# Performance work log

Measured on AMD Instinct MI355X. Metric: run time of the kernel, lower is better.

Reference implementation:

```python
import jax, jax.numpy as jnp
import numpy as np

D_MODEL = 1024
NHEAD = 16
HEAD_DIM = D_MODEL // NHEAD
B, T = 2, 2048


def setup_inputs() -> dict:
    key = jax.random.key(0)
    ks = jax.random.split(key, 11)
    s = 1.0 / np.sqrt(D_MODEL)
    inp = {
        'q': jax.random.normal(ks[0], (B, T, D_MODEL), jnp.float32),
        'k': jax.random.normal(ks[1], (B, T, D_MODEL), jnp.float32),
        'v': jax.random.normal(ks[2], (B, T, D_MODEL), jnp.float32),
        'Wq': jax.random.normal(ks[3], (D_MODEL, D_MODEL), jnp.float32) * s,
        'bq': jnp.zeros((D_MODEL,), jnp.float32),
        'Wk': jax.random.normal(ks[4], (D_MODEL, D_MODEL), jnp.float32) * s,
        'bk': jnp.zeros((D_MODEL,), jnp.float32),
        'Wv': jax.random.normal(ks[5], (D_MODEL, D_MODEL), jnp.float32) * s,
        'bv': jnp.zeros((D_MODEL,), jnp.float32),
        'Wo': jax.random.normal(ks[6], (D_MODEL, D_MODEL), jnp.float32) * s,
        'bo': jnp.zeros((D_MODEL,), jnp.float32),
    }
    return inp


def reference(q, k, v, Wq, bq, Wk, bk, Wv, bv, Wo, bo):
    scale = np.sqrt(HEAD_DIM).astype(np.float32)
    # projections (torch Linear: x @ W.T + b), split heads -> [B, H, T, Dh]
    def proj(x, W, b):
        y = jnp.einsum('btd,ed->bte', x, W) + b
        return y.reshape(B, T, NHEAD, HEAD_DIM).transpose(0, 2, 1, 3)
    qh = proj(q, Wq, bq)
    kh = proj(k, Wk, bk)
    vh = proj(v, Wv, bv)
    scores = jnp.einsum('bhqd,bhkd->bhqk', qh, kh) / scale  # [B,H,T,T]
    weights = jax.nn.softmax(scores, axis=-1)
    out = jnp.einsum('bhqk,bhkd->bhqd', weights, vh)        # [B,H,T,Dh]
    out = out.transpose(0, 2, 1, 3).reshape(B, T, D_MODEL)
    return jnp.einsum('btd,ed->bte', out, Wo) + bo
```

## Files before the change

kernel.cpp:

```cpp
#include <hip/hip_runtime.h>
#include <cstdint>
#include <cstddef>


#define D_MODEL 1024
#define NHEAD   16
#define HDIM    64
#define BATCH   2
#define SEQ     2048
#define BT      (BATCH * SEQ)

#define QSCALE 0.18033688011112043f

typedef __bf16 bf16;
typedef __bf16 bf16x8 __attribute__((ext_vector_type(8)));
typedef __bf16 bf16x4 __attribute__((ext_vector_type(4)));
typedef float  floatx4 __attribute__((ext_vector_type(4)));
typedef short  short4v __attribute__((ext_vector_type(4)));

#define MFMA16(a, b, c) __builtin_amdgcn_mfma_f32_16x16x32_bf16((a), (b), (c), 0, 0, 0)

__device__ __forceinline__ floatx4 MFMA16B(bf16x4 a, bf16x4 b, floatx4 c) {
  return __builtin_amdgcn_mfma_f32_16x16x16bf16_1k(
      __builtin_bit_cast(short4v, a), __builtin_bit_cast(short4v, b), c, 0, 0, 0);
}

__device__ __forceinline__ float fexp2(float x) {
  return __builtin_amdgcn_exp2f(x);
}

__device__ __forceinline__ void async_cp16(const bf16* g, bf16* l) {
  __builtin_amdgcn_global_load_lds(
      (__attribute__((address_space(1))) void*)(g),
      (__attribute__((address_space(3))) void*)(l), 16, 0, 0);
}

__global__ __launch_bounds__(256) void cvt7(
    const float* __restrict__ s0, const float* __restrict__ s1,
    const float* __restrict__ s2, const float* __restrict__ s3,
    const float* __restrict__ s4, const float* __restrict__ s5,
    const float* __restrict__ s6,
    bf16* __restrict__ d0, bf16* __restrict__ d1, bf16* __restrict__ d2,
    bf16* __restrict__ d3, bf16* __restrict__ d4, bf16* __restrict__ d5,
    bf16* __restrict__ d6)
{
  const float* src; bf16* dst; int n4;
  switch (blockIdx.y) {
    case 0:  src = s0; dst = d0; n4 = (BT * D_MODEL) / 4; break;
    case 1:  src = s1; dst = d1; n4 = (BT * D_MODEL) / 4; break;
    case 2:  src = s2; dst = d2; n4 = (BT * D_MODEL) / 4; break;
    case 3:  src = s3; dst = d3; n4 = (D_MODEL * D_MODEL) / 4; break;
    case 4:  src = s4; dst = d4; n4 = (D_MODEL * D_MODEL) / 4; break;
    case 5:  src = s5; dst = d5; n4 = (D_MODEL * D_MODEL) / 4; break;
    default: src = s6; dst = d6; n4 = (D_MODEL * D_MODEL) / 4; break;
  }
  int stride = gridDim.x * blockDim.x;
  for (int i = blockIdx.x * blockDim.x + threadIdx.x; i < n4; i += stride) {
    float4 f = ((const float4*)src)[i];
    bf16x4 h;
    h[0] = (bf16)f.x; h[1] = (bf16)f.y; h[2] = (bf16)f.z; h[3] = (bf16)f.w;
    ((bf16x4*)dst)[i] = h;
  }
}

__device__ __forceinline__ void gemm128_core(
    const bf16* __restrict__ A, const bf16* __restrict__ W,
    int m0, int n0, bf16* As, bf16* Bs, floatx4 acc[4][4])
{
  const int t = threadIdx.x;
  const int l = t & 63, w = t >> 6;
  const int quad = l >> 4, lr = l & 15;
  const int wm = (w >> 1) * 64, wn = (w & 1) * 64;

  floatx4 z = {0.f, 0.f, 0.f, 0.f};
#pragma unroll
  for (int i = 0; i < 4; i++)
#pragma unroll
    for (int j = 0; j < 4; j++) acc[i][j] = z;

  for (int kt = 0; kt < 1024; kt += 32) {
    __syncthreads();
#pragma unroll
    for (int i = 0; i < 2; i++) {
      int c = i * 256 + t;
      int row = c >> 2, ci = c & 3;
      async_cp16(A + (size_t)(m0 + row) * 1024 + kt + ci * 8,
                 As + (i * 256 + w * 64) * 8);
      async_cp16(W + (size_t)(n0 + row) * 1024 + kt + ci * 8,
                 Bs + (i * 256 + w * 64) * 8);
    }
    __syncthreads();

    bf16x8 af[4], bfr[4];
#pragma unroll
    for (int i = 0; i < 4; i++) {
      af[i]  = *(const bf16x8*)(As + (wm + i * 16 + lr) * 32 + quad * 8);
      bfr[i] = *(const bf16x8*)(Bs + (wn + i * 16 + lr) * 32 + quad * 8);
    }
#pragma unroll
    for (int i = 0; i < 4; i++)
#pragma unroll
      for (int j = 0; j < 4; j++)
        acc[i][j] = MFMA16(af[i], bfr[j], acc[i][j]);
  }
}

__global__ __launch_bounds__(256) void qkv_gemm(
    const bf16* __restrict__ qb, const bf16* __restrict__ kb, const bf16* __restrict__ vb,
    const bf16* __restrict__ wq, const bf16* __restrict__ wk, const bf16* __restrict__ wv,
    const float* __restrict__ biasq, const float* __restrict__ biask, const float* __restrict__ biasv,
    bf16* __restrict__ qh, bf16* __restrict__ kh, bf16* __restrict__ vt)
{
  __shared__ bf16 As[128 * 32];
  __shared__ bf16 Bs[128 * 32];
  const int zid = blockIdx.z;
  const bf16* A = (zid == 0) ? qb : ((zid == 1) ? kb : vb);
  const bf16* W = (zid == 0) ? wq : ((zid == 1) ? wk : wv);
  const float* bias = (zid == 0) ? biasq : ((zid == 1) ? biask : biasv);
  const int m0 = blockIdx.x * 128, n0 = blockIdx.y * 128;

  floatx4 acc[4][4];
  gemm128_core(A, W, m0, n0, As, Bs, acc);

  const int t = threadIdx.x, l = t & 63, w = t >> 6;
  const int quad = l >> 4, lr = l & 15;
  const int wm = (w >> 1) * 64, wn = (w & 1) * 64;
  const float sc = (zid == 0) ? QSCALE : 1.0f;

  if (zid < 2) {
    bf16* out = (zid == 0) ? qh : kh;
#pragma unroll
    for (int i = 0; i < 4; i++) {
      int mbase = m0 + wm + i * 16 + quad * 4;
      int b  = mbase >> 11;
      int tq = mbase & 2047;
#pragma unroll
      for (int j = 0; j < 4; j++) {
        int n = n0 + wn + j * 16 + lr;
        float bv = bias[n];
        int h = n >> 6, dh = n & 63;
        bf16* p = out + ((size_t)((b * NHEAD + h) * SEQ + tq)) * HDIM + dh;
#pragma unroll
        for (int r = 0; r < 4; r++)
          p[(size_t)r * HDIM] = (bf16)((acc[i][j][r] + bv) * sc);
      }
    }
  } else {
#pragma unroll
    for (int i = 0; i < 4; i++) {
      int mbase = m0 + wm + i * 16 + quad * 4;
      int b  = mbase >> 11;
      int tq = mbase & 2047;
#pragma unroll
      for (int j = 0; j < 4; j++) {
        int n = n0 + wn + j * 16 + lr;
        float bv = bias[n];
        int h = n >> 6, dh = n & 63;
        bf16x4 pk;
#pragma unroll
        for (int r = 0; r < 4; r++) pk[r] = (bf16)(acc[i][j][r] + bv);
        *(bf16x4*)(vt + ((size_t)((b * NHEAD + h) * HDIM + dh)) * SEQ + tq) = pk;
      }
    }
  }
}

__global__ __launch_bounds__(256, 2) void attn_fused(
    const bf16* __restrict__ qh, const bf16* __restrict__ kh,
    const bf16* __restrict__ vt, bf16* __restrict__ attn)
{
  __shared__ __align__(16) char smem[65536];

  const int t = threadIdx.x, l = t & 63, w = t >> 6;
  const int quad = l >> 4, lr = l & 15;
  const int bh = blockIdx.y;
  const int qt0 = blockIdx.x * 128;
  const bf16* qg = qh + (size_t)bh * SEQ * HDIM;
  const bf16* kg = kh + (size_t)bh * SEQ * HDIM;
  const bf16* vg = vt + (size_t)bh * HDIM * SEQ;

  const bf16* kseg[4];
  const bf16* vseg[4];
#pragma unroll
  for (int i = 0; i < 4; i++) {
    int s = w * 4 + i;
    int krow = s * 8 + (l >> 3);
    kseg[i] = kg + (size_t)krow * HDIM + (((l & 7) ^ (l >> 3)) * 8);
    int vrow = s * 4 + (l >> 4);
    vseg[i] = vg + (size_t)vrow * SEQ + (((l & 15) ^ (vrow & 15)) * 8);
  }

  bf16x8 qf[2][2];
#pragma unroll
  for (int g = 0; g < 2; g++)
#pragma unroll
    for (int ko = 0; ko < 2; ko++)
      qf[g][ko] = *(const bf16x8*)(qg + (size_t)(qt0 + w * 32 + g * 16 + lr) * HDIM
                                   + ko * 32 + quad * 8);

  const floatx4 zz = {0.f, 0.f, 0.f, 0.f};
  floatx4 Oacc[2][4];
#pragma unroll
  for (int g = 0; g < 2; g++)
#pragma unroll
    for (int dt = 0; dt < 4; dt++) Oacc[g][dt] = zz;
  float mrow[2] = {-3.0e38f, -3.0e38f};
  float lrow[2] = {0.f, 0.f};

  auto stage = [&](int buf, int kt) {
    bf16* Kb = (bf16*)(smem + buf * 32768);
    bf16* Vb = (bf16*)(smem + buf * 32768 + 16384);
    int off = kt * 128;
#pragma unroll
    for (int i = 0; i < 4; i++) {
      async_cp16(kseg[i] + (size_t)off * HDIM, Kb + (w * 4 + i) * 512);
      async_cp16(vseg[i] + off,                Vb + (w * 4 + i) * 512);
    }
  };

  stage(0, 0);

  for (int kt = 0; kt < 16; kt++) {
    const int p = kt & 1;
    __syncthreads();
    if (kt + 1 < 16) stage(1 - p, kt + 1);
    const bf16* Ks  = (const bf16*)(smem + p * 32768);
    const bf16* Vts = (const bf16*)(smem + p * 32768 + 16384);

    const bf16* krow0 = Ks + lr * 64 + ((quad ^ (lr & 7)) * 8);
    const bf16* krow1 = Ks + lr * 64 + (((quad + 4) ^ (lr & 7)) * 8);

    floatx4 s0[8], s1[8];
#pragma unroll
    for (int ni = 0; ni < 8; ni++) {
      bf16x8 k0 = *(const bf16x8*)(krow0 + ni * 1024);
      bf16x8 k1 = *(const bf16x8*)(krow1 + ni * 1024);
      floatx4 a0 = MFMA16(k0, qf[0][0], zz);
      a0 = MFMA16(k1, qf[0][1], a0);
      floatx4 a1 = MFMA16(k0, qf[1][0], zz);
      a1 = MFMA16(k1, qf[1][1], a1);
      s0[ni] = a0;
      s1[ni] = a1;
    }

    bf16x4 pk0[8], pk1[8];
#pragma unroll
    for (int g = 0; g < 2; g++) {
      floatx4* sg = g ? s1 : s0;
      bf16x4* pkg = g ? pk1 : pk0;
      float rmax = sg[0][0];
#pragma unroll
      for (int ni = 0; ni < 8; ni++)
#pragma unroll
        for (int r = 0; r < 4; r++) rmax = fmaxf(rmax, sg[ni][r]);
      rmax = fmaxf(rmax, __shfl_xor(rmax, 16, 64));
      rmax = fmaxf(rmax, __shfl_xor(rmax, 32, 64));
      if (!__all(rmax - mrow[g] <= 8.0f)) {
        float mnew = fmaxf(mrow[g], rmax);
        float al = fexp2(mrow[g] - mnew);
        mrow[g] = mnew;
        lrow[g] *= al;
#pragma unroll
        for (int dt = 0; dt < 4; dt++)
#pragma unroll
          for (int r = 0; r < 4; r++) Oacc[g][dt][r] *= al;
      }
      float m = mrow[g];
      float rsum = 0.f;
#pragma unroll
      for (int ni = 0; ni < 8; ni++)
#pragma unroll
        for (int r = 0; r < 4; r++) {
          float pv = fexp2(sg[ni][r] - m);
          rsum += pv;
          pkg[ni][r] = (bf16)pv;
        }
      rsum += __shfl_xor(rsum, 16, 64);
      rsum += __shfl_xor(rsum, 32, 64);
      lrow[g] += rsum;
    }

    const bf16* vbase = Vts + lr * 128 + (quad & 1) * 4;
#pragma unroll
    for (int ni = 0; ni < 8; ni++) {
      const bf16* vp = vbase + (((ni * 2 + (quad >> 1)) ^ lr) * 8);
#pragma unroll
      for (int dt = 0; dt < 4; dt++) {
        bf16x4 vf = *(const bf16x4*)(vp + dt * 2048);
        Oacc[0][dt] = MFMA16B(vf, pk0[ni], Oacc[0][dt]);
        Oacc[1][dt] = MFMA16B(vf, pk1[ni], Oacc[1][dt]);
      }
    }
  }

  bf16* Ost = (bf16*)smem;
#pragma unroll
  for (int g = 0; g < 2; g++) {
    float inv = 1.0f / lrow[g];
#pragma unroll
    for (int dt = 0; dt < 4; dt++) {
      bf16x4 ov;
#pragma unroll
      for (int r = 0; r < 4; r++) ov[r] = (bf16)(Oacc[g][dt][r] * inv);
      *(bf16x4*)(Ost + (size_t)(w * 32 + g * 16 + lr) * 72 + dt * 16 + quad * 4) = ov;
    }
  }
  __syncthreads();

  const int b = bh >> 4, h = bh & 15;
#pragma unroll
  for (int i = 0; i < 4; i++) {
    int c = t + 256 * i;
    int row = c >> 3, ci = c & 7;
    *(int4*)(attn + ((size_t)b * SEQ + qt0 + row) * D_MODEL + h * HDIM + ci * 8) =
        *(const int4*)(Ost + row * 72 + ci * 8);
  }
}

__global__ __launch_bounds__(256) void oproj_gemm(
    const bf16* __restrict__ attn, const bf16* __restrict__ wo,
    const float* __restrict__ bo, float* __restrict__ out)
{
  __shared__ bf16 As[64 * 32];
  __shared__ bf16 Bs[64 * 32];
  const int m0 = blockIdx.x * 64, n0 = blockIdx.y * 64;
  const int t = threadIdx.x, l = t & 63, w = t >> 6;
  const int quad = l >> 4, lr = l & 15;
  const int wm = (w >> 1) * 32, wn = (w & 1) * 32;

  floatx4 z = {0.f, 0.f, 0.f, 0.f};
  floatx4 acc[2][2];
#pragma unroll
  for (int i = 0; i < 2; i++)
#pragma unroll
    for (int j = 0; j < 2; j++) acc[i][j] = z;

  for (int kt = 0; kt < 1024; kt += 32) {
    __syncthreads();
    {
      int row = t >> 2, ci = t & 3;
      async_cp16(attn + (size_t)(m0 + row) * 1024 + kt + ci * 8,
                 As + (w * 64) * 8);
      async_cp16(wo + (size_t)(n0 + row) * 1024 + kt + ci * 8,
                 Bs + (w * 64) * 8);
    }
    __syncthreads();

    bf16x8 af[2], bfr[2];
#pragma unroll
    for (int i = 0; i < 2; i++) {
      af[i]  = *(const bf16x8*)(As + (wm + i * 16 + lr) * 32 + quad * 8);
      bfr[i] = *(const bf16x8*)(Bs + (wn + i * 16 + lr) * 32 + quad * 8);
    }
#pragma unroll
    for (int i = 0; i < 2; i++)
#pragma unroll
      for (int j = 0; j < 2; j++)
        acc[i][j] = MFMA16(af[i], bfr[j], acc[i][j]);
  }

#pragma unroll
  for (int i = 0; i < 2; i++) {
    int m = m0 + wm + i * 16 + quad * 4;
#pragma unroll
    for (int j = 0; j < 2; j++) {
      int n = n0 + wn + j * 16 + lr;
      float bv = bo[n];
      float* p = out + (size_t)m * D_MODEL + n;
#pragma unroll
      for (int r = 0; r < 4; r++)
        p[(size_t)r * D_MODEL] = acc[i][j][r] + bv;
    }
  }
}

extern "C" void kernel_launch(void* const* d_in, const int* in_sizes, int n_in,
                              void* d_out, int out_size, void* d_ws, size_t ws_size,
                              hipStream_t stream)
{
  const float* q  = (const float*)d_in[0];
  const float* k  = (const float*)d_in[1];
  const float* v  = (const float*)d_in[2];
  const float* Wq = (const float*)d_in[3];
  const float* bq = (const float*)d_in[4];
  const float* Wk = (const float*)d_in[5];
  const float* bk = (const float*)d_in[6];
  const float* Wv = (const float*)d_in[7];
  const float* bv = (const float*)d_in[8];
  const float* Wo = (const float*)d_in[9];
  const float* bo = (const float*)d_in[10];

  const size_t NQ = (size_t)BT * D_MODEL;
  const size_t NW = (size_t)D_MODEL * D_MODEL;

  bf16* p = (bf16*)d_ws;
  bf16* qb   = p; p += NQ;
  bf16* kb   = p; p += NQ;
  bf16* vb   = p; p += NQ;
  bf16* wqb  = p; p += NW;
  bf16* wkb  = p; p += NW;
  bf16* wvb  = p; p += NW;
  bf16* wob  = p; p += NW;
  bf16* qhp  = p; p += NQ;
  bf16* khp  = p; p += NQ;
  bf16* vtp  = p; p += NQ;
  bf16* attn = p; p += NQ;

  cvt7<<<dim3(1024, 7, 1), 256, 0, stream>>>(q, k, v, Wq, Wk, Wv, Wo,
                                             qb, kb, vb, wqb, wkb, wvb, wob);
  qkv_gemm<<<dim3(32, 8, 3), 256, 0, stream>>>(qb, kb, vb, wqb, wkb, wvb,
                                               bq, bk, bv, qhp, khp, vtp);
  attn_fused<<<dim3(16, 32, 1), 256, 0, stream>>>(qhp, khp, vtp, attn);
  oproj_gemm<<<dim3(64, 16, 1), 256, 0, stream>>>(attn, wob, bo, (float*)d_out);
}
```

Baseline: 223.6 us.

## Remap attention blocks across heads, tree-reduce softmax, enlarge oproj M tile

The attention kernel remaps block indices so concurrently scheduled blocks spread over different batch-heads, which may change L2/cache locality. The softmax max and sum reductions become tree-shaped instead of serial chains, and the MFMA and V-load order is interleaved to shorten dependency chains. The output projection GEMM doubles its M tile to 128, so each wave computes 4x2 MFMA tiles, reusing B fragments and halving the grid. Together these aim to cut instruction latency and load traffic, at the cost of more registers and fewer blocks in the projection kernel.

```diff
diff --git a/kernel.cpp b/kernel.cpp
--- a/kernel.cpp
+++ b/kernel.cpp
@@ -173,8 +173,12 @@
 
   const int t = threadIdx.x, l = t & 63, w = t >> 6;
   const int quad = l >> 4, lr = l & 15;
-  const int bh = blockIdx.y;
-  const int qt0 = blockIdx.x * 128;
+
+  const int hb  = blockIdx.y * 16 + blockIdx.x;
+  const int j   = hb >> 3;
+  const int bh  = (hb & 7) + ((j & 3) << 3);
+  const int qt0 = (j >> 2) * 128;
+
   const bf16* qg = qh + (size_t)bh * SEQ * HDIM;
   const bf16* kg = kh + (size_t)bh * SEQ * HDIM;
   const bf16* vg = vt + (size_t)bh * HDIM * SEQ;
@@ -236,8 +240,8 @@
       bf16x8 k0 = *(const bf16x8*)(krow0 + ni * 1024);
       bf16x8 k1 = *(const bf16x8*)(krow1 + ni * 1024);
       floatx4 a0 = MFMA16(k0, qf[0][0], zz);
+      floatx4 a1 = MFMA16(k0, qf[1][0], zz);
       a0 = MFMA16(k1, qf[0][1], a0);
-      floatx4 a1 = MFMA16(k0, qf[1][0], zz);
       a1 = MFMA16(k1, qf[1][1], a1);
       s0[ni] = a0;
       s1[ni] = a1;
@@ -248,13 +252,16 @@
     for (int g = 0; g < 2; g++) {
       floatx4* sg = g ? s1 : s0;
       bf16x4* pkg = g ? pk1 : pk0;
-      float rmax = sg[0][0];
+
+      float xm[8];
 #pragma unroll
       for (int ni = 0; ni < 8; ni++)
-#pragma unroll
-        for (int r = 0; r < 4; r++) rmax = fmaxf(rmax, sg[ni][r]);
+        xm[ni] = fmaxf(fmaxf(sg[ni][0], sg[ni][1]), fmaxf(sg[ni][2], sg[ni][3]));
+      float rmax = fmaxf(fmaxf(fmaxf(xm[0], xm[1]), fmaxf(xm[2], xm[3])),
+                         fmaxf(fmaxf(xm[4], xm[5]), fmaxf(xm[6], xm[7])));
       rmax = fmaxf(rmax, __shfl_xor(rmax, 16, 64));
       rmax = fmaxf(rmax, __shfl_xor(rmax, 32, 64));
+
       if (!__all(rmax - mrow[g] <= 8.0f)) {
         float mnew = fmaxf(mrow[g], rmax);
         float al = fexp2(mrow[g] - mnew);
@@ -265,16 +272,19 @@
 #pragma unroll
           for (int r = 0; r < 4; r++) Oacc[g][dt][r] *= al;
       }
-      float m = mrow[g];
-      float rsum = 0.f;
-#pragma unroll
-      for (int ni = 0; ni < 8; ni++)
-#pragma unroll
-        for (int r = 0; r < 4; r++) {
-          float pv = fexp2(sg[ni][r] - m);
-          rsum += pv;
-          pkg[ni][r] = (bf16)pv;
-        }
+
+      const float m = mrow[g];
+      float tt[8];
+#pragma unroll
+      for (int ni = 0; ni < 8; ni++) {
+        float p0 = fexp2(sg[ni][0] - m), p1 = fexp2(sg[ni][1] - m);
+        float p2 = fexp2(sg[ni][2] - m), p3 = fexp2(sg[ni][3] - m);
+        pkg[ni][0] = (bf16)p0; pkg[ni][1] = (bf16)p1;
+        pkg[ni][2] = (bf16)p2; pkg[ni][3] = (bf16)p3;
+        tt[ni] = (p0 + p1) + (p2 + p3);
+      }
+      float rsum = ((tt[0] + tt[1]) + (tt[2] + tt[3]))
+                 + ((tt[4] + tt[5]) + (tt[6] + tt[7]));
       rsum += __shfl_xor(rsum, 16, 64);
       rsum += __shfl_xor(rsum, 32, 64);
       lrow[g] += rsum;
@@ -284,12 +294,18 @@
 #pragma unroll
     for (int ni = 0; ni < 8; ni++) {
       const bf16* vp = vbase + (((ni * 2 + (quad >> 1)) ^ lr) * 8);
-#pragma unroll
-      for (int dt = 0; dt < 4; dt++) {
-        bf16x4 vf = *(const bf16x4*)(vp + dt * 2048);
-        Oacc[0][dt] = MFMA16B(vf, pk0[ni], Oacc[0][dt]);
-        Oacc[1][dt] = MFMA16B(vf, pk1[ni], Oacc[1][dt]);
-      }
+      bf16x4 vf0 = *(const bf16x4*)(vp);
+      bf16x4 vf1 = *(const bf16x4*)(vp + 2048);
+      bf16x4 vf2 = *(const bf16x4*)(vp + 4096);
+      bf16x4 vf3 = *(const bf16x4*)(vp + 6144);
+      Oacc[0][0] = MFMA16B(vf0, pk0[ni], Oacc[0][0]);
+      Oacc[1][0] = MFMA16B(vf0, pk1[ni], Oacc[1][0]);
+      Oacc[0][1] = MFMA16B(vf1, pk0[ni], Oacc[0][1]);
+      Oacc[1][1] = MFMA16B(vf1, pk1[ni], Oacc[1][1]);
+      Oacc[0][2] = MFMA16B(vf2, pk0[ni], Oacc[0][2]);
+      Oacc[1][2] = MFMA16B(vf2, pk1[ni], Oacc[1][2]);
+      Oacc[0][3] = MFMA16B(vf3, pk0[ni], Oacc[0][3]);
+      Oacc[1][3] = MFMA16B(vf3, pk1[ni], Oacc[1][3]);
     }
   }
 
@@ -321,46 +337,52 @@
     const bf16* __restrict__ attn, const bf16* __restrict__ wo,
     const float* __restrict__ bo, float* __restrict__ out)
 {
-  __shared__ bf16 As[64 * 32];
+  __shared__ bf16 As[128 * 32];
   __shared__ bf16 Bs[64 * 32];
-  const int m0 = blockIdx.x * 64, n0 = blockIdx.y * 64;
+  const int m0 = blockIdx.x * 128, n0 = blockIdx.y * 64;
   const int t = threadIdx.x, l = t & 63, w = t >> 6;
   const int quad = l >> 4, lr = l & 15;
-  const int wm = (w >> 1) * 32, wn = (w & 1) * 32;
+  const int wm = (w >> 1) * 64, wn = (w & 1) * 32;
 
   floatx4 z = {0.f, 0.f, 0.f, 0.f};
-  floatx4 acc[2][2];
-#pragma unroll
-  for (int i = 0; i < 2; i++)
+  floatx4 acc[4][2];
+#pragma unroll
+  for (int i = 0; i < 4; i++)
 #pragma unroll
     for (int j = 0; j < 2; j++) acc[i][j] = z;
 
   for (int kt = 0; kt < 1024; kt += 32) {
     __syncthreads();
+#pragma unroll
+    for (int i = 0; i < 2; i++) {
+      int c = i * 256 + t;
+      int row = c >> 2, ci = c & 3;
+      async_cp16(attn + (size_t)(m0 + row) * 1024 + kt + ci * 8,
+                 As + (i * 256 + w * 64) * 8);
+    }
     {
       int row = t >> 2, ci = t & 3;
-      async_cp16(attn + (size_t)(m0 + row) * 1024 + kt + ci * 8,
-                 As + (w * 64) * 8);
       async_cp16(wo + (size_t)(n0 + row) * 1024 + kt + ci * 8,
                  Bs + (w * 64) * 8);
     }
     __syncthreads();
 
-    bf16x8 af[2], bfr[2];
-#pragma unroll
-    for (int i = 0; i < 2; i++) {
+    bf16x8 af[4], bfr[2];
+#pragma unroll
+    for (int i = 0; i < 4; i++)
       af[i]  = *(const bf16x8*)(As + (wm + i * 16 + lr) * 32 + quad * 8);
-      bfr[i] = *(const bf16x8*)(Bs + (wn + i * 16 + lr) * 32 + quad * 8);
-    }
-#pragma unroll
-    for (int i = 0; i < 2; i++)
+#pragma unroll
+    for (int j = 0; j < 2; j++)
+      bfr[j] = *(const bf16x8*)(Bs + (wn + j * 16 + lr) * 32 + quad * 8);
+#pragma unroll
+    for (int i = 0; i < 4; i++)
 #pragma unroll
       for (int j = 0; j < 2; j++)
         acc[i][j] = MFMA16(af[i], bfr[j], acc[i][j]);
   }
 
 #pragma unroll
-  for (int i = 0; i < 2; i++) {
+  for (int i = 0; i < 4; i++) {
     int m = m0 + wm + i * 16 + quad * 4;
 #pragma unroll
     for (int j = 0; j < 2; j++) {
@@ -411,5 +433,5 @@
   qkv_gemm<<<dim3(32, 8, 3), 256, 0, stream>>>(qb, kb, vb, wqb, wkb, wvb,
                                                bq, bk, bv, qhp, khp, vtp);
   attn_fused<<<dim3(16, 32, 1), 256, 0, stream>>>(qhp, khp, vtp, attn);
-  oproj_gemm<<<dim3(64, 16, 1), 256, 0, stream>>>(attn, wob, bo, (float*)d_out);
-}
+  oproj_gemm<<<dim3(32, 16, 1), 256, 0, stream>>>(attn, wob, bo, (float*)d_out);
+}
```

After: 224.8 us. About the same (+0.6%).
